# Optimization experiments

Hardware: AMD Instinct MI355X
Metric: run time of the kernel (lower is better)

Reference implementation:

```python
import jax, jax.numpy as jnp
import numpy as np

UNITS = 1024
FORECAST = 128
FEATS = 128
BATCH = 256
WARMUP = 256


def setup_inputs() -> dict:
    key = jax.random.key(0)
    ks = jax.random.split(key, 4)
    s = 0.02  # small init scale to keep gates out of saturation
    return {
        "inputs": jax.random.normal(ks[0], (BATCH, WARMUP, FEATS), jnp.float32),
        "W_i": jax.random.normal(ks[1], (FEATS, 4 * UNITS), jnp.float32) * s,
        "W_h": jax.random.normal(ks[2], (UNITS, 4 * UNITS), jnp.float32) * s,
        "b": jnp.zeros((4 * UNITS,), jnp.float32),
        "W_d": jax.random.normal(ks[3], (UNITS, FEATS), jnp.float32) * s,
        "b_d": jnp.zeros((FEATS,), jnp.float32),
    }


def _lstm_cell(x, h, c, W_i, W_h, b):
    # Keras LSTMCell: gates ordered [input, forget, cell-candidate, output]
    z = x @ W_i + h @ W_h + b  # [B, 4U]
    i, f, g, o = jnp.split(z, 4, axis=-1)
    c_new = jax.nn.sigmoid(f) * c + jax.nn.sigmoid(i) * jnp.tanh(g)
    h_new = jax.nn.sigmoid(o) * jnp.tanh(c_new)
    return h_new, c_new


def reference(inputs, W_i, W_h, b, W_d, b_d):
    B = inputs.shape[0]
    U = W_h.shape[0]
    h0 = jnp.zeros((B, U), inputs.dtype)
    c0 = jnp.zeros((B, U), inputs.dtype)

    # warmup: run LSTM over the input sequence, keep final state
    def warm_step(carry, x_t):
        h, c = carry
        h, c = _lstm_cell(x_t, h, c, W_i, W_h, b)
        return (h, c), None

    (h, c), _ = jax.lax.scan(warm_step, (h0, c0), jnp.swapaxes(inputs, 0, 1))
    pred = h @ W_d + b_d  # first prediction [B, F]

    def fc_step(carry, _):
        h, c, p = carry
        h, c = _lstm_cell(p, h, c, W_i, W_h, b)
        p = h @ W_d + b_d
        return (h, c, p), p

    _, preds_rest = jax.lax.scan(fc_step, (h, c, pred), None, length=FORECAST - 1)
    preds = jnp.concatenate([pred[None], preds_rest], axis=0)  # [T, B, F]
    return jnp.swapaxes(preds, 0, 1)  # [B, T, F]
```

## Files before the change

kernel.cpp:

```cpp
#include <hip/hip_runtime.h>
#include <hip/hip_bf16.h>

#define UNITS 1024
#define FEATS 128
#define NG    4096
#define NSTEP 383
#define HS    262144
#define HSB   524288UL

#define OX   0UL
#define OWH  16777216UL
#define OWI  25165824UL
#define OWF  26214400UL
#define OWD  34603008UL
#define OBR  34865152UL
#define OBF  34881536UL
#define OH0  34897920UL
#define OHP  35422208UL
#define OHC  36470784UL
#define OCNT 68452352UL

typedef __attribute__((ext_vector_type(8))) short bf16x8;
typedef __attribute__((ext_vector_type(4))) float f32x4;
typedef __attribute__((ext_vector_type(4))) int i32x4;
typedef __attribute__((address_space(3))) char lds_char;
typedef __attribute__((address_space(1))) const char glb_char;

__device__ __forceinline__ void gload_lds16(const void* g, void* l) {
    __builtin_amdgcn_global_load_lds((glb_char*)g, (lds_char*)l, 16, 0, 0);
}
__device__ __forceinline__ int llc_load(const int* p) {
    int v;
    asm volatile("global_load_dword %0, %1, off sc0 sc1\n\ts_waitcnt vmcnt(0)"
                 : "=v"(v) : "v"(p) : "memory");
    return v;
}
__device__ __forceinline__ void l2_atomic_inc(int* p) {
    int one = 1;
    asm volatile("global_atomic_add %0, %1, off" :: "v"(p), "v"(one) : "memory");
}
__device__ __forceinline__ int l2_atomic_poll(int* p) {
    int v; int zero = 0;
    asm volatile("global_atomic_add %0, %1, %2, off sc0\n\ts_waitcnt vmcnt(0)"
                 : "=v"(v) : "v"(p), "v"(zero) : "memory");
    return v;
}

#define CFENCE asm volatile("" ::: "memory")
#define VMCNT0 asm volatile("s_waitcnt vmcnt(0)" ::: "memory")
#define L1INV  asm volatile("buffer_inv" ::: "memory")

__device__ __forceinline__ float sigf(float x) { return 1.0f / (1.0f + __expf(-x)); }
__device__ __forceinline__ float tanh_fast(float x) { return 2.0f / (1.0f + __expf(-2.0f * x)) - 1.0f; }

__device__ __forceinline__ int PK(int k) {
    return (k & ~15) | ((k & 3) << 2) | ((k >> 2) & 3);
}

__device__ __forceinline__ __hip_bfloat16* hist_ptr(char* ws, int s) {
    size_t off;
    if (s == 0)        off = OH0;
    else if (s <= 32)  off = OX  + (size_t)(s - 1) * HSB;
    else if (s <= 48)  off = OWH + (size_t)(s - 33) * HSB;
    else if (s <= 50)  off = OWI + (size_t)(s - 49) * HSB;
    else if (s <= 111) off = OHC + (size_t)(s - 51) * HSB;
    else               off = OWF + (size_t)(s - 112) * HSB;
    return (__hip_bfloat16*)(ws + off);
}

__device__ __forceinline__ void llc_sync(int* c, int target) {
    CFENCE;
    __syncthreads();
    if (threadIdx.x == 0) {
        atomicAdd(c, 1);
        while (llc_load(c) < target) __builtin_amdgcn_s_sleep(8);
    }
    __syncthreads();
    CFENCE;
}


__global__ void cvt_bf16(const float* __restrict__ in, __hip_bfloat16* __restrict__ out, int n) {
    int i = (blockIdx.x * blockDim.x + threadIdx.x) * 4;
    if (i >= n) return;
    float4 v = *(const float4*)(in + i);
    union { ushort4 u4; __hip_bfloat16 h[4]; } pk;
    pk.h[0] = __float2bfloat16(v.x);
    pk.h[1] = __float2bfloat16(v.y);
    pk.h[2] = __float2bfloat16(v.z);
    pk.h[3] = __float2bfloat16(v.w);
    *(ushort4*)(out + i) = pk.u4;
}

__global__ void build_whwi(const float* __restrict__ Wh, const float* __restrict__ Wi,
                           __hip_bfloat16* __restrict__ WhR, __hip_bfloat16* __restrict__ WiR) {
    int idx = blockIdx.x * 256 + threadIdx.x;
    int k = idx >> 12, col = idx & 4095;
    int j = ((col & 1023) << 2) | (col >> 10);
    if (k < 1024) WhR[(size_t)j * 1024 + k] = __float2bfloat16(Wh[(size_t)PK(k) * 4096 + col]);
    else          WiR[(size_t)j * 128 + (k - 1024)] = __float2bfloat16(Wi[(size_t)(k - 1024) * 4096 + col]);
}

__global__ void build_wd(const float* __restrict__ Wd, __hip_bfloat16* __restrict__ WdT) {
    int idx = blockIdx.x * 256 + threadIdx.x;
    int f = idx >> 10, k = idx & 1023;
    WdT[(size_t)f * 1024 + k] = __float2bfloat16(Wd[(size_t)PK(k) * 128 + f]);
}

__global__ void build_bias(const float* __restrict__ b, const float* __restrict__ bd,
                           const float* __restrict__ Wi, float* __restrict__ br, float* __restrict__ bf) {
    int j = blockIdx.x * 256 + threadIdx.x;
    int col = ((j & 3) << 10) | (j >> 2);
    float base = b[col];
    br[j] = base;
    float v = base;
    for (int q = 0; q < 128; ++q) v += bd[q] * Wi[(size_t)q * 4096 + col];
    bf[j] = v;
}

__global__ __launch_bounds__(256) void build_wf(const __hip_bfloat16* __restrict__ WhR,
                                                const __hip_bfloat16* __restrict__ WiR,
                                                const float* __restrict__ Wd,
                                                __hip_bfloat16* __restrict__ WfR) {
    const int j0 = blockIdx.x * 64, k0 = blockIdx.y * 64;
    const int tid = threadIdx.x, wave = tid >> 6, lane = tid & 63;
    const int wj = (wave >> 1) * 32, wk = (wave & 1) * 32;
    const int lr = lane & 15, lq = lane >> 4;
    const int TL = ((lr & 3) << 2) | (lr >> 2);
    f32x4 acc[2][2] = {};
    #pragma unroll
    for (int kc = 0; kc < 4; ++kc) {
        bf16x8 dfr[2], ifr[2];
        #pragma unroll
        for (int q2 = 0; q2 < 2; ++q2) {
            const float* p = Wd + (size_t)(k0 + wk + q2 * 16 + TL) * 128 + kc * 32 + lq * 8;
            __hip_bfloat16* dp = (__hip_bfloat16*)&dfr[q2];
            #pragma unroll
            for (int e = 0; e < 8; ++e) dp[e] = __float2bfloat16(p[e]);
            ifr[q2] = *(const bf16x8*)(WiR + (size_t)(j0 + wj + q2 * 16 + lr) * 128 + kc * 32 + lq * 8);
        }
        acc[0][0] = __builtin_amdgcn_mfma_f32_16x16x32_bf16(dfr[0], ifr[0], acc[0][0], 0, 0, 0);
        acc[0][1] = __builtin_amdgcn_mfma_f32_16x16x32_bf16(dfr[0], ifr[1], acc[0][1], 0, 0, 0);
        acc[1][0] = __builtin_amdgcn_mfma_f32_16x16x32_bf16(dfr[1], ifr[0], acc[1][0], 0, 0, 0);
        acc[1][1] = __builtin_amdgcn_mfma_f32_16x16x32_bf16(dfr[1], ifr[1], acc[1][1], 0, 0, 0);
    }
    #pragma unroll
    for (int cf = 0; cf < 2; ++cf)
        #pragma unroll
        for (int rf = 0; rf < 2; ++rf) {
            const int k = k0 + wk + cf * 16 + lq * 4;
            const int j = j0 + wj + rf * 16 + lr;
            const __hip_bfloat16* whp = WhR + (size_t)j * 1024 + k;
            __hip_bfloat16* wfp = WfR + (size_t)j * 1024 + k;
            #pragma unroll
            for (int e = 0; e < 4; ++e)
                wfp[e] = __float2bfloat16(acc[cf][rf][e] + __bfloat162float(whp[e]));
        }
}

__global__ __launch_bounds__(512, 2) void persist(char* ws) {
    const __hip_bfloat16* xb  = (const __hip_bfloat16*)(ws + OX);
    const __hip_bfloat16* whg = (const __hip_bfloat16*)(ws + OWH);
    const __hip_bfloat16* wig = (const __hip_bfloat16*)(ws + OWI);
    const __hip_bfloat16* wfg = (const __hip_bfloat16*)(ws + OWF);
    const float* brg = (const float*)(ws + OBR);
    const float* bfg = (const float*)(ws + OBF);
    __hip_bfloat16* hp0 = (__hip_bfloat16*)(ws + OHP);
    __hip_bfloat16* hp1 = hp0 + HS;

    __shared__ __hip_bfloat16 Als[9][32][128];
    __shared__ float Xl[4][2][4][2][256];
    __shared__ __hip_bfloat16 hTile[32][32];
    __shared__ int claimv[2];
    __shared__ int rdy[16];

    const int tid = threadIdx.x;

    if (tid < 16) rdy[tid] = 0;
    if (tid == 0) {
        unsigned xcd;
        asm volatile("s_getreg_b32 %0, hwreg(HW_REG_XCC_ID, 0, 32)" : "=s"(xcd));
        int* slotc = (int*)(ws + OCNT + 8192);
        int slot = atomicAdd(slotc + (xcd & 7), 1);
        claimv[0] = (int)(xcd & 7);
        claimv[1] = slot & 31;
    }
    __syncthreads();
    const int grp  = claimv[0];
    const int tile = claimv[1];
    const int n0 = tile * 128;
    const int b0 = grp * 32;
    const int ublk = tile * 32;
    int* fbase = (int*)(ws + OCNT + (size_t)grp * 1024);
    int* glc   = (int*)(ws + OCNT + 8320);

    const int wave = tid >> 6, lane = tid & 63;
    const int cq = wave & 1, kh = wave >> 1;
    const int lr = lane & 15, lq = lane >> 4;

    bf16x8 w[4][9];
    #pragma unroll
    for (int tc = 0; tc < 4; ++tc) {
        const size_t row = (size_t)(n0 + cq * 64 + tc * 16 + lr);
        w[tc][0] = *(const bf16x8*)(wig + row * 128 + kh * 32 + lq * 8);
        #pragma unroll
        for (int c = 0; c < 8; ++c)
            w[tc][1 + c] = *(const bf16x8*)(whg + row * 1024 + c * 128 + kh * 32 + lq * 8);
    }
    float4 biasq = *(const float4*)(brg + n0 + cq * 64 + kh * 16 + lq * 4);

    float creg[2] = {0.f, 0.f};

    if (wave == 0) {
        #pragma unroll
        for (int j = 0; j < 8; ++j) {
            const int r32 = j * 4 + lq;
            const int ce = ((lane & 15) ^ (r32 & 15)) << 3;
            gload_lds16(xb + (size_t)(b0 + r32) * 32768 + ce,
                        (char*)&Als[0][0][0] + j * 1024);
        }
    }

    for (int t = 0; t < NSTEP; ++t) {
        const bool fc = (t >= 256);
        const __hip_bfloat16* hsrc = fc ? hist_ptr(ws, t - 256) : ((t & 1) ? hp1 : hp0);
        __hip_bfloat16* hdst = (t >= 255) ? hist_ptr(ws, t - 255) : ((t & 1) ? hp0 : hp1);

        if (t == 256) {
            #pragma unroll
            for (int tc = 0; tc < 4; ++tc) {
                const size_t row = (size_t)(n0 + cq * 64 + tc * 16 + lr);
                #pragma unroll
                for (int c = 0; c < 8; ++c)
                    w[tc][1 + c] = *(const bf16x8*)(wfg + row * 1024 + c * 128 + kh * 32 + lq * 8);
            }
            biasq = *(const float4*)(bfg + n0 + cq * 64 + kh * 16 + lq * 4);
            VMCNT0;
            llc_sync(glc, 256);
        }

        if (t > 0 && lane == 0) {
            int* fl = fbase + wave * 32;
            while (l2_atomic_poll(fl) < 4 * t) __builtin_amdgcn_s_sleep(1);
        }
        L1INV;
        {
            const __hip_bfloat16* srcb = hsrc + (size_t)b0 * 1024 + wave * 128;
            char* dstc = (char*)&Als[1 + wave][0][0];
            #pragma unroll
            for (int j = 0; j < 8; ++j) {
                const int r32 = j * 4 + lq;
                const int ce = ((lane & 15) ^ (r32 & 15)) << 3;
                gload_lds16(srcb + (size_t)r32 * 1024 + ce, dstc + j * 1024);
            }
        }
        VMCNT0;
        __hip_atomic_store(&rdy[wave], t + 1, __ATOMIC_RELEASE, __HIP_MEMORY_SCOPE_WORKGROUP);

        f32x4 acc[4][2] = {};
        const int sc = ((kh * 4 + lq) ^ lr);
        auto wr_ = [&](int p) {
            while (__hip_atomic_load(&rdy[p], __ATOMIC_ACQUIRE, __HIP_MEMORY_SCOPE_WORKGROUP) < t + 1) {}
            __builtin_amdgcn_sched_barrier(0);
        };
        auto mfr = [&](int r) {
            const bf16x8 a0 = *(const bf16x8*)&Als[r][lr][sc * 8];
            const bf16x8 a1 = *(const bf16x8*)&Als[r][lr + 16][sc * 8];
            #pragma unroll
            for (int tc = 0; tc < 4; ++tc) {
                acc[tc][0] = __builtin_amdgcn_mfma_f32_16x16x32_bf16(w[tc][r], a0, acc[tc][0], 0, 0, 0);
                acc[tc][1] = __builtin_amdgcn_mfma_f32_16x16x32_bf16(w[tc][r], a1, acc[tc][1], 0, 0, 0);
            }
        };
        if (!fc) { wr_(0); mfr(0); }
        #pragma unroll
        for (int r = 1; r <= 8; ++r) { wr_(r - 1); mfr(r); }

        #pragma unroll
        for (int tc = 0; tc < 4; ++tc)
            #pragma unroll
            for (int rf = 0; rf < 2; ++rf)
                *(f32x4*)&Xl[kh][cq][tc][rf][lane * 4] = acc[tc][rf];
        __syncthreads();
        #pragma unroll
        for (int rf = 0; rf < 2; ++rf) {
            f32x4 z = {0.f, 0.f, 0.f, 0.f};
            #pragma unroll
            for (int k2 = 0; k2 < 4; ++k2)
                z += *(const f32x4*)&Xl[k2][cq][kh][rf][lane * 4];
            const float zi = z[0] + biasq.x;
            const float zf = z[1] + biasq.y;
            const float zg = z[2] + biasq.z;
            const float zo = z[3] + biasq.w;
            const float cn = sigf(zf) * creg[rf] + sigf(zi) * tanh_fast(zg);
            creg[rf] = cn;
            hTile[rf * 16 + lr][cq * 16 + lq * 4 + kh] = __float2bfloat16(sigf(zo) * tanh_fast(cn));
        }
        __syncthreads();

        if (tid < 128) {
            const int bl = tid >> 2, ch = tid & 3;
            *(i32x4*)(hdst + (size_t)(b0 + bl) * 1024 + ublk + ch * 8) =
                *(const i32x4*)&hTile[bl][ch * 8];
        }
        VMCNT0;
        __syncthreads();
        if (tid == 0) l2_atomic_inc(fbase + (tile >> 2) * 32);

        if (wave == 0 && t + 1 < 256) {
            #pragma unroll
            for (int j = 0; j < 8; ++j) {
                const int r32 = j * 4 + lq;
                const int ce = ((lane & 15) ^ (r32 & 15)) << 3;
                gload_lds16(xb + (size_t)(b0 + r32) * 32768 + (size_t)(t + 1) * 128 + ce,
                            (char*)&Als[0][0][0] + j * 1024);
            }
        }
    }
}

__global__ __launch_bounds__(256) void pgemm(char* ws, float* __restrict__ out,
                                             const float* __restrict__ bd) {
    const int t = blockIdx.x >> 2;
    const int r0 = (blockIdx.x & 3) * 64;
    const int f0 = blockIdx.y * 64;
    const __hip_bfloat16* A = hist_ptr(ws, t);
    const __hip_bfloat16* Bw = (const __hip_bfloat16*)(ws + OWD);

    __shared__ __hip_bfloat16 Al[2][64 * 64];
    __shared__ __hip_bfloat16 Bl[2][64 * 64];

    const int tid = threadIdx.x;
    const int wave = tid >> 6, lane = tid & 63;
    const int whb = (wave >> 1) * 32, wcf = (wave & 1) * 32;
    const int lr = lane & 15, lq = lane >> 4;
    const int l8 = lane >> 3, cb = lane & 7;
    const int gsw = ((cb ^ l8) << 3);
    const int xk = lr & 7;

    f32x4 acc[2][2] = {};
    const int rA0 = whb + lr, rA1 = whb + lr + 16;
    const int rB0 = wcf + lr, rB1 = wcf + lr + 16;

    auto stage = [&](int buf, int k0) {
        #pragma unroll
        for (int l = 0; l < 2; ++l) {
            const int rt = wave * 16 + l * 8;
            const int row = rt + l8;
            gload_lds16(A + (size_t)(r0 + row) * 1024 + k0 + gsw, &Al[buf][rt * 64]);
            gload_lds16(Bw + (size_t)(f0 + row) * 1024 + k0 + gsw, &Bl[buf][rt * 64]);
        }
    };

    stage(0, 0);
    for (int kk = 0; kk < 16; ++kk) {
        const int buf = kk & 1;
        if (kk + 1 < 16) { stage(buf ^ 1, (kk + 1) << 6); asm volatile("s_waitcnt vmcnt(4)" ::: "memory"); }
        else             { VMCNT0; }
        CFENCE; __builtin_amdgcn_s_barrier(); CFENCE;
        #pragma unroll
        for (int ks = 0; ks < 2; ++ks) {
            const int g0 = ((ks * 4 + lq) ^ xk) << 3;
            bf16x8 a0 = *(const bf16x8*)&Al[buf][rA0 * 64 + g0];
            bf16x8 a1 = *(const bf16x8*)&Al[buf][rA1 * 64 + g0];
            bf16x8 w0 = *(const bf16x8*)&Bl[buf][rB0 * 64 + g0];
            bf16x8 w1 = *(const bf16x8*)&Bl[buf][rB1 * 64 + g0];
            acc[0][0] = __builtin_amdgcn_mfma_f32_16x16x32_bf16(w0, a0, acc[0][0], 0, 0, 0);
            acc[0][1] = __builtin_amdgcn_mfma_f32_16x16x32_bf16(w0, a1, acc[0][1], 0, 0, 0);
            acc[1][0] = __builtin_amdgcn_mfma_f32_16x16x32_bf16(w1, a0, acc[1][0], 0, 0, 0);
            acc[1][1] = __builtin_amdgcn_mfma_f32_16x16x32_bf16(w1, a1, acc[1][1], 0, 0, 0);
        }
        CFENCE; __builtin_amdgcn_s_barrier(); CFENCE;
    }
    #pragma unroll
    for (int cf = 0; cf < 2; ++cf) {
        const int fb = f0 + wcf + cf * 16 + lq * 4;
        const float4 b4 = *(const float4*)(bd + fb);
        #pragma unroll
        for (int rf = 0; rf < 2; ++rf) {
            const int b = r0 + whb + rf * 16 + lr;
            float4 o;
            o.x = acc[cf][rf][0] + b4.x;
            o.y = acc[cf][rf][1] + b4.y;
            o.z = acc[cf][rf][2] + b4.z;
            o.w = acc[cf][rf][3] + b4.w;
            *(float4*)(out + (size_t)b * 16384 + (size_t)t * 128 + fb) = o;
        }
    }
}


extern "C" void kernel_launch(void* const* d_in, const int* in_sizes, int n_in,
                              void* d_out, int out_size, void* d_ws, size_t ws_size,
                              hipStream_t stream) {
    const float* inputs = (const float*)d_in[0];
    const float* W_i    = (const float*)d_in[1];
    const float* W_h    = (const float*)d_in[2];
    const float* b      = (const float*)d_in[3];
    const float* W_d    = (const float*)d_in[4];
    const float* b_d    = (const float*)d_in[5];
    float* out = (float*)d_out;
    char* ws = (char*)d_ws;

    (void)hipMemsetAsync(ws + OHP, 0, HSB, stream);
    (void)hipMemsetAsync(ws + OCNT, 0, 16384, stream);

    cvt_bf16<<<8192, 256, 0, stream>>>(inputs, (__hip_bfloat16*)(ws + OX), 256 * 256 * 128);
    build_whwi<<<(1152 * 4096) / 256, 256, 0, stream>>>(
        W_h, W_i, (__hip_bfloat16*)(ws + OWH), (__hip_bfloat16*)(ws + OWI));
    build_wd<<<(128 * 1024) / 256, 256, 0, stream>>>(W_d, (__hip_bfloat16*)(ws + OWD));
    build_bias<<<16, 256, 0, stream>>>(b, b_d, W_i, (float*)(ws + OBR), (float*)(ws + OBF));
    build_wf<<<dim3(64, 16), 256, 0, stream>>>(
        (const __hip_bfloat16*)(ws + OWH), (const __hip_bfloat16*)(ws + OWI),
        W_d, (__hip_bfloat16*)(ws + OWF));

    char* wsp = ws;
    void* ka[] = { &wsp };
    (void)hipLaunchCooperativeKernel((void*)persist, dim3(256), dim3(512), ka, 0, stream);

    pgemm<<<dim3(512, 2), 256, 0, stream>>>(ws, out, b_d);
}
```

Measured before the change: 1.758 ms.

## Split each batch tile into two 16-row halves with separate flags to pipeline

Each workgroup's 32 batch rows are processed as two 16-row halves, each with its own LDS buffer, readiness flags and global completion counters. The second half's hidden-state loads overlap with compute on the first half, and each half's h slice is published as soon as it is done. The x input is now loaded inside the step rather than prefetched a step ahead. The change adds more flag polling, another barrier pair per step and smaller MFMA batches per LDS read, and it reorganizes the counter layout.

Result: slower. 2.735 ms (+55.6%).

```diff
diff --git a/kernel.cpp b/kernel.cpp
--- a/kernel.cpp
+++ b/kernel.cpp
@@ -168,15 +168,15 @@
     __hip_bfloat16* hp0 = (__hip_bfloat16*)(ws + OHP);
     __hip_bfloat16* hp1 = hp0 + HS;
 
-    __shared__ __hip_bfloat16 Als[9][32][128];
-    __shared__ float Xl[4][2][4][2][256];
-    __shared__ __hip_bfloat16 hTile[32][32];
+    __shared__ __hip_bfloat16 Als[2][9][16][128];
+    __shared__ float Xl[4][2][4][256];
+    __shared__ __hip_bfloat16 hTile[2][16][32];
     __shared__ int claimv[2];
-    __shared__ int rdy[16];
+    __shared__ int rdy[2][8];
 
     const int tid = threadIdx.x;
 
-    if (tid < 16) rdy[tid] = 0;
+    if (tid < 16) rdy[tid >> 3][tid & 7] = 0;
     if (tid == 0) {
         unsigned xcd;
         asm volatile("s_getreg_b32 %0, hwreg(HW_REG_XCC_ID, 0, 32)" : "=s"(xcd));
@@ -208,18 +208,10 @@
             w[tc][1 + c] = *(const bf16x8*)(whg + row * 1024 + c * 128 + kh * 32 + lq * 8);
     }
     float4 biasq = *(const float4*)(brg + n0 + cq * 64 + kh * 16 + lq * 4);
-
     float creg[2] = {0.f, 0.f};
 
-    if (wave == 0) {
-        #pragma unroll
-        for (int j = 0; j < 8; ++j) {
-            const int r32 = j * 4 + lq;
-            const int ce = ((lane & 15) ^ (r32 & 15)) << 3;
-            gload_lds16(xb + (size_t)(b0 + r32) * 32768 + ce,
-                        (char*)&Als[0][0][0] + j * 1024);
-        }
-    }
+    const int sr = lane >> 4;
+    const int scol = lane & 15;
 
     for (int t = 0; t < NSTEP; ++t) {
         const bool fc = (t >= 256);
@@ -240,80 +232,112 @@
         }
 
         if (t > 0 && lane == 0) {
-            int* fl = fbase + wave * 32;
-            while (l2_atomic_poll(fl) < 4 * t) __builtin_amdgcn_s_sleep(1);
+            int* f0 = fbase + wave * 16;
+            while (l2_atomic_poll(f0) < 4 * t) __builtin_amdgcn_s_sleep(1);
         }
         L1INV;
         {
-            const __hip_bfloat16* srcb = hsrc + (size_t)b0 * 1024 + wave * 128;
-            char* dstc = (char*)&Als[1 + wave][0][0];
-            #pragma unroll
-            for (int j = 0; j < 8; ++j) {
-                const int r32 = j * 4 + lq;
-                const int ce = ((lane & 15) ^ (r32 & 15)) << 3;
-                gload_lds16(srcb + (size_t)r32 * 1024 + ce, dstc + j * 1024);
-            }
-        }
+            const int b0g = b0;
+            if (!fc && wave == 0) {
+                #pragma unroll
+                for (int j = 0; j < 4; ++j) {
+                    const int row = j * 4 + sr;
+                    const int ce = (scol ^ row) << 3;
+                    gload_lds16(xb + (size_t)(b0g + row) * 32768 + (size_t)t * 128 + ce,
+                                (char*)&Als[0][0][0][0] + j * 1024);
+                }
+            }
+            const __hip_bfloat16* srcb = hsrc + (size_t)b0g * 1024 + wave * 128;
+            #pragma unroll
+            for (int j = 0; j < 4; ++j) {
+                const int row = j * 4 + sr;
+                const int ce = (scol ^ row) << 3;
+                gload_lds16(srcb + (size_t)row * 1024 + ce,
+                            (char*)&Als[0][1 + wave][0][0] + j * 1024);
+            }
+        }
+        if (t > 0 && lane == 0) {
+            int* f1 = fbase + (8 + wave) * 16;
+            while (l2_atomic_poll(f1) < 4 * t) __builtin_amdgcn_s_sleep(1);
+        }
+        {
+            const int b0g = b0 + 16;
+            if (!fc && wave == 0) {
+                #pragma unroll
+                for (int j = 0; j < 4; ++j) {
+                    const int row = j * 4 + sr;
+                    const int ce = (scol ^ row) << 3;
+                    gload_lds16(xb + (size_t)(b0g + row) * 32768 + (size_t)t * 128 + ce,
+                                (char*)&Als[1][0][0][0] + j * 1024);
+                }
+            }
+            const __hip_bfloat16* srcb = hsrc + (size_t)b0g * 1024 + wave * 128;
+            #pragma unroll
+            for (int j = 0; j < 4; ++j) {
+                const int row = j * 4 + sr;
+                const int ce = (scol ^ row) << 3;
+                gload_lds16(srcb + (size_t)row * 1024 + ce,
+                            (char*)&Als[1][1 + wave][0][0] + j * 1024);
+            }
+        }
+        if (wave == 0 && !fc) { asm volatile("s_waitcnt vmcnt(8)" ::: "memory"); }
+        else                  { asm volatile("s_waitcnt vmcnt(4)" ::: "memory"); }
+        __hip_atomic_store(&rdy[0][wave], t + 1, __ATOMIC_RELEASE, __HIP_MEMORY_SCOPE_WORKGROUP);
         VMCNT0;
-        __hip_atomic_store(&rdy[wave], t + 1, __ATOMIC_RELEASE, __HIP_MEMORY_SCOPE_WORKGROUP);
-
-        f32x4 acc[4][2] = {};
+        __hip_atomic_store(&rdy[1][wave], t + 1, __ATOMIC_RELEASE, __HIP_MEMORY_SCOPE_WORKGROUP);
+
         const int sc = ((kh * 4 + lq) ^ lr);
-        auto wr_ = [&](int p) {
-            while (__hip_atomic_load(&rdy[p], __ATOMIC_ACQUIRE, __HIP_MEMORY_SCOPE_WORKGROUP) < t + 1) {}
-            __builtin_amdgcn_sched_barrier(0);
-        };
-        auto mfr = [&](int r) {
-            const bf16x8 a0 = *(const bf16x8*)&Als[r][lr][sc * 8];
-            const bf16x8 a1 = *(const bf16x8*)&Als[r][lr + 16][sc * 8];
-            #pragma unroll
-            for (int tc = 0; tc < 4; ++tc) {
-                acc[tc][0] = __builtin_amdgcn_mfma_f32_16x16x32_bf16(w[tc][r], a0, acc[tc][0], 0, 0, 0);
-                acc[tc][1] = __builtin_amdgcn_mfma_f32_16x16x32_bf16(w[tc][r], a1, acc[tc][1], 0, 0, 0);
-            }
-        };
-        if (!fc) { wr_(0); mfr(0); }
-        #pragma unroll
-        for (int r = 1; r <= 8; ++r) { wr_(r - 1); mfr(r); }
-
-        #pragma unroll
-        for (int tc = 0; tc < 4; ++tc)
-            #pragma unroll
-            for (int rf = 0; rf < 2; ++rf)
-                *(f32x4*)&Xl[kh][cq][tc][rf][lane * 4] = acc[tc][rf];
-        __syncthreads();
-        #pragma unroll
-        for (int rf = 0; rf < 2; ++rf) {
-            f32x4 z = {0.f, 0.f, 0.f, 0.f};
-            #pragma unroll
-            for (int k2 = 0; k2 < 4; ++k2)
-                z += *(const f32x4*)&Xl[k2][cq][kh][rf][lane * 4];
-            const float zi = z[0] + biasq.x;
-            const float zf = z[1] + biasq.y;
-            const float zg = z[2] + biasq.z;
-            const float zo = z[3] + biasq.w;
-            const float cn = sigf(zf) * creg[rf] + sigf(zi) * tanh_fast(zg);
-            creg[rf] = cn;
-            hTile[rf * 16 + lr][cq * 16 + lq * 4 + kh] = __float2bfloat16(sigf(zo) * tanh_fast(cn));
-        }
-        __syncthreads();
-
-        if (tid < 128) {
-            const int bl = tid >> 2, ch = tid & 3;
-            *(i32x4*)(hdst + (size_t)(b0 + bl) * 1024 + ublk + ch * 8) =
-                *(const i32x4*)&hTile[bl][ch * 8];
-        }
-        VMCNT0;
-        __syncthreads();
-        if (tid == 0) l2_atomic_inc(fbase + (tile >> 2) * 32);
-
-        if (wave == 0 && t + 1 < 256) {
-            #pragma unroll
-            for (int j = 0; j < 8; ++j) {
-                const int r32 = j * 4 + lq;
-                const int ce = ((lane & 15) ^ (r32 & 15)) << 3;
-                gload_lds16(xb + (size_t)(b0 + r32) * 32768 + (size_t)(t + 1) * 128 + ce,
-                            (char*)&Als[0][0][0] + j * 1024);
+
+        #pragma unroll
+        for (int g = 0; g < 2; ++g) {
+            {
+                volatile int* vr = &rdy[g][0];
+                for (;;) {
+                    int m = vr[0];
+                    #pragma unroll
+                    for (int i = 1; i < 8; ++i) { int u = vr[i]; m = (u < m) ? u : m; }
+                    if (m >= t + 1) break;
+                }
+                __builtin_amdgcn_sched_barrier(0);
+            }
+            f32x4 acc[4] = {};
+            if (!fc) {
+                const bf16x8 a = *(const bf16x8*)&Als[g][0][lr][sc * 8];
+                #pragma unroll
+                for (int tc = 0; tc < 4; ++tc)
+                    acc[tc] = __builtin_amdgcn_mfma_f32_16x16x32_bf16(w[tc][0], a, acc[tc], 0, 0, 0);
+            }
+            #pragma unroll
+            for (int r = 1; r <= 8; ++r) {
+                const bf16x8 a = *(const bf16x8*)&Als[g][r][lr][sc * 8];
+                #pragma unroll
+                for (int tc = 0; tc < 4; ++tc)
+                    acc[tc] = __builtin_amdgcn_mfma_f32_16x16x32_bf16(w[tc][r], a, acc[tc], 0, 0, 0);
+            }
+            #pragma unroll
+            for (int tc = 0; tc < 4; ++tc)
+                *(f32x4*)&Xl[kh][cq][tc][lane * 4] = acc[tc];
+            __syncthreads();
+            {
+                f32x4 z = *(const f32x4*)&Xl[0][cq][kh][lane * 4];
+                #pragma unroll
+                for (int k2 = 1; k2 < 4; ++k2)
+                    z += *(const f32x4*)&Xl[k2][cq][kh][lane * 4];
+                const float zi = z[0] + biasq.x;
+                const float zf = z[1] + biasq.y;
+                const float zg = z[2] + biasq.z;
+                const float zo = z[3] + biasq.w;
+                const float cn = sigf(zf) * creg[g] + sigf(zi) * tanh_fast(zg);
+                creg[g] = cn;
+                hTile[g][lr][cq * 16 + lq * 4 + kh] = __float2bfloat16(sigf(zo) * tanh_fast(cn));
+            }
+            __syncthreads();
+            if (wave == g) {
+                const int row = lane >> 2, ch = lane & 3;
+                *(i32x4*)(hdst + (size_t)(b0 + g * 16 + row) * 1024 + ublk + ch * 8) =
+                    *(const i32x4*)&hTile[g][row][ch * 8];
+                VMCNT0;
+                if (lane == 0) l2_atomic_inc(fbase + (g * 8 + (tile >> 2)) * 16);
             }
         }
     }
```

## Give each wave full-K gate rows to drop cross-wave LDS reduction

Applied to the files above, without the earlier changes.

Each wave now owns 16 gate rows across the entire K dimension, so it holds 36 weight fragments and accumulates the full dot product in registers. This removes the Xl LDS partial-sum buffer and one workgroup barrier per step. hTile is double-buffered so a single wave can publish h and bump the flag without a trailing barrier. The x-input load moves into the current step and gets its own ready flag, and the spin-wait sleep is removed. The cost is higher register pressure, serialised publishing by one wave, and busier polling.

After: 2.095 ms. 19.2% more time.

```diff
diff --git a/kernel.cpp b/kernel.cpp
--- a/kernel.cpp
+++ b/kernel.cpp
@@ -169,14 +169,13 @@
     __hip_bfloat16* hp1 = hp0 + HS;
 
     __shared__ __hip_bfloat16 Als[9][32][128];
-    __shared__ float Xl[4][2][4][2][256];
-    __shared__ __hip_bfloat16 hTile[32][32];
+    __shared__ __hip_bfloat16 hTile[2][32][32];
     __shared__ int claimv[2];
-    __shared__ int rdy[16];
+    __shared__ int rdy[12];
 
     const int tid = threadIdx.x;
 
-    if (tid < 16) rdy[tid] = 0;
+    if (tid < 12) rdy[tid] = 0;
     if (tid == 0) {
         unsigned xcd;
         asm volatile("s_getreg_b32 %0, hwreg(HW_REG_XCC_ID, 0, 32)" : "=s"(xcd));
@@ -195,31 +194,24 @@
     int* glc   = (int*)(ws + OCNT + 8320);
 
     const int wave = tid >> 6, lane = tid & 63;
-    const int cq = wave & 1, kh = wave >> 1;
     const int lr = lane & 15, lq = lane >> 4;
 
-    bf16x8 w[4][9];
+    const size_t wrow = (size_t)(n0 + wave * 16 + lr);
+    bf16x8 wv[36];
     #pragma unroll
-    for (int tc = 0; tc < 4; ++tc) {
-        const size_t row = (size_t)(n0 + cq * 64 + tc * 16 + lr);
-        w[tc][0] = *(const bf16x8*)(wig + row * 128 + kh * 32 + lq * 8);
-        #pragma unroll
-        for (int c = 0; c < 8; ++c)
-            w[tc][1 + c] = *(const bf16x8*)(whg + row * 1024 + c * 128 + kh * 32 + lq * 8);
-    }
-    float4 biasq = *(const float4*)(brg + n0 + cq * 64 + kh * 16 + lq * 4);
-
+    for (int s = 0; s < 4; ++s)
+        wv[s] = *(const bf16x8*)(wig + wrow * 128 + s * 32 + lq * 8);
+    #pragma unroll
+    for (int c = 0; c < 8; ++c)
+        #pragma unroll
+        for (int s = 0; s < 4; ++s)
+            wv[4 + 4 * c + s] = *(const bf16x8*)(whg + wrow * 1024 + c * 128 + s * 32 + lq * 8);
+    float4 biasq = *(const float4*)(brg + n0 + wave * 16 + lq * 4);
     float creg[2] = {0.f, 0.f};
 
-    if (wave == 0) {
-        #pragma unroll
-        for (int j = 0; j < 8; ++j) {
-            const int r32 = j * 4 + lq;
-            const int ce = ((lane & 15) ^ (r32 & 15)) << 3;
-            gload_lds16(xb + (size_t)(b0 + r32) * 32768 + ce,
-                        (char*)&Als[0][0][0] + j * 1024);
-        }
-    }
+    const int sr = lane >> 4;
+    const int scol = lane & 15;
+    const int upos = ((wave >> 2) << 4) | (lq << 2) | (wave & 3);
 
     for (int t = 0; t < NSTEP; ++t) {
         const bool fc = (t >= 256);
@@ -228,20 +220,18 @@
 
         if (t == 256) {
             #pragma unroll
-            for (int tc = 0; tc < 4; ++tc) {
-                const size_t row = (size_t)(n0 + cq * 64 + tc * 16 + lr);
+            for (int c = 0; c < 8; ++c)
                 #pragma unroll
-                for (int c = 0; c < 8; ++c)
-                    w[tc][1 + c] = *(const bf16x8*)(wfg + row * 1024 + c * 128 + kh * 32 + lq * 8);
-            }
-            biasq = *(const float4*)(bfg + n0 + cq * 64 + kh * 16 + lq * 4);
+                for (int s = 0; s < 4; ++s)
+                    wv[4 + 4 * c + s] = *(const bf16x8*)(wfg + wrow * 1024 + c * 128 + s * 32 + lq * 8);
+            biasq = *(const float4*)(bfg + n0 + wave * 16 + lq * 4);
             VMCNT0;
             llc_sync(glc, 256);
         }
 
         if (t > 0 && lane == 0) {
             int* fl = fbase + wave * 32;
-            while (l2_atomic_poll(fl) < 4 * t) __builtin_amdgcn_s_sleep(1);
+            while (l2_atomic_poll(fl) < 4 * t) { }
         }
         L1INV;
         {
@@ -249,72 +239,82 @@
             char* dstc = (char*)&Als[1 + wave][0][0];
             #pragma unroll
             for (int j = 0; j < 8; ++j) {
-                const int r32 = j * 4 + lq;
-                const int ce = ((lane & 15) ^ (r32 & 15)) << 3;
-                gload_lds16(srcb + (size_t)r32 * 1024 + ce, dstc + j * 1024);
-            }
-        }
-        VMCNT0;
-        __hip_atomic_store(&rdy[wave], t + 1, __ATOMIC_RELEASE, __HIP_MEMORY_SCOPE_WORKGROUP);
-
-        f32x4 acc[4][2] = {};
-        const int sc = ((kh * 4 + lq) ^ lr);
-        auto wr_ = [&](int p) {
-            while (__hip_atomic_load(&rdy[p], __ATOMIC_ACQUIRE, __HIP_MEMORY_SCOPE_WORKGROUP) < t + 1) {}
+                const int row = j * 4 + sr;
+                const int ce = (scol ^ (row & 15)) << 3;
+                gload_lds16(srcb + (size_t)row * 1024 + ce, dstc + j * 1024);
+            }
+        }
+        if (wave == 0) {
+            if (!fc) {
+                #pragma unroll
+                for (int j = 0; j < 8; ++j) {
+                    const int row = j * 4 + sr;
+                    const int ce = (scol ^ (row & 15)) << 3;
+                    gload_lds16(xb + (size_t)(b0 + row) * 32768 + (size_t)t * 128 + ce,
+                                (char*)&Als[0][0][0] + j * 1024);
+                }
+                asm volatile("s_waitcnt vmcnt(8)" ::: "memory");
+                __hip_atomic_store(&rdy[0], t + 1, __ATOMIC_RELEASE, __HIP_MEMORY_SCOPE_WORKGROUP);
+                VMCNT0;
+                __hip_atomic_store(&rdy[8], t + 1, __ATOMIC_RELEASE, __HIP_MEMORY_SCOPE_WORKGROUP);
+            } else {
+                VMCNT0;
+                __hip_atomic_store(&rdy[0], t + 1, __ATOMIC_RELEASE, __HIP_MEMORY_SCOPE_WORKGROUP);
+            }
+        } else {
+            VMCNT0;
+            __hip_atomic_store(&rdy[wave], t + 1, __ATOMIC_RELEASE, __HIP_MEMORY_SCOPE_WORKGROUP);
+        }
+
+        f32x4 acc[2][2] = {};
+        auto gate = [&](int idx) {
+            while (__hip_atomic_load(&rdy[idx], __ATOMIC_ACQUIRE, __HIP_MEMORY_SCOPE_WORKGROUP) < t + 1) {}
             __builtin_amdgcn_sched_barrier(0);
         };
-        auto mfr = [&](int r) {
-            const bf16x8 a0 = *(const bf16x8*)&Als[r][lr][sc * 8];
-            const bf16x8 a1 = *(const bf16x8*)&Als[r][lr + 16][sc * 8];
-            #pragma unroll
-            for (int tc = 0; tc < 4; ++tc) {
-                acc[tc][0] = __builtin_amdgcn_mfma_f32_16x16x32_bf16(w[tc][r], a0, acc[tc][0], 0, 0, 0);
-                acc[tc][1] = __builtin_amdgcn_mfma_f32_16x16x32_bf16(w[tc][r], a1, acc[tc][1], 0, 0, 0);
+        auto chunk = [&](int r, int wbase) {
+            #pragma unroll
+            for (int s = 0; s < 4; ++s) {
+                const int sc = ((s * 4 + lq) ^ lr) << 3;
+                const bf16x8 a0 = *(const bf16x8*)&Als[r][lr][sc];
+                const bf16x8 a1 = *(const bf16x8*)&Als[r][lr + 16][sc];
+                acc[0][s & 1] = __builtin_amdgcn_mfma_f32_16x16x32_bf16(wv[wbase + s], a0, acc[0][s & 1], 0, 0, 0);
+                acc[1][s & 1] = __builtin_amdgcn_mfma_f32_16x16x32_bf16(wv[wbase + s], a1, acc[1][s & 1], 0, 0, 0);
             }
         };
-        if (!fc) { wr_(0); mfr(0); }
-        #pragma unroll
-        for (int r = 1; r <= 8; ++r) { wr_(r - 1); mfr(r); }
-
-        #pragma unroll
-        for (int tc = 0; tc < 4; ++tc)
-            #pragma unroll
-            for (int rf = 0; rf < 2; ++rf)
-                *(f32x4*)&Xl[kh][cq][tc][rf][lane * 4] = acc[tc][rf];
+        #pragma unroll
+        for (int c = 0; c < 8; ++c) { gate(c); chunk(1 + c, 4 + 4 * c); }
+        if (!fc) { gate(8); chunk(0, 0); }
+
+        {
+            const f32x4 z0 = acc[0][0] + acc[0][1];
+            const f32x4 z1 = acc[1][0] + acc[1][1];
+            {
+                const float zi = z0[0] + biasq.x, zf = z0[1] + biasq.y;
+                const float zg = z0[2] + biasq.z, zo = z0[3] + biasq.w;
+                const float cn = sigf(zf) * creg[0] + sigf(zi) * tanh_fast(zg);
+                creg[0] = cn;
+                hTile[t & 1][lr][upos] = __float2bfloat16(sigf(zo) * tanh_fast(cn));
+            }
+            {
+                const float zi = z1[0] + biasq.x, zf = z1[1] + biasq.y;
+                const float zg = z1[2] + biasq.z, zo = z1[3] + biasq.w;
+                const float cn = sigf(zf) * creg[1] + sigf(zi) * tanh_fast(zg);
+                creg[1] = cn;
+                hTile[t & 1][16 + lr][upos] = __float2bfloat16(sigf(zo) * tanh_fast(cn));
+            }
+        }
         __syncthreads();
-        #pragma unroll
-        for (int rf = 0; rf < 2; ++rf) {
-            f32x4 z = {0.f, 0.f, 0.f, 0.f};
-            #pragma unroll
-            for (int k2 = 0; k2 < 4; ++k2)
-                z += *(const f32x4*)&Xl[k2][cq][kh][rf][lane * 4];
-            const float zi = z[0] + biasq.x;
-            const float zf = z[1] + biasq.y;
-            const float zg = z[2] + biasq.z;
-            const float zo = z[3] + biasq.w;
-            const float cn = sigf(zf) * creg[rf] + sigf(zi) * tanh_fast(zg);
-            creg[rf] = cn;
-            hTile[rf * 16 + lr][cq * 16 + lq * 4 + kh] = __float2bfloat16(sigf(zo) * tanh_fast(cn));
-        }
-        __syncthreads();
-
-        if (tid < 128) {
-            const int bl = tid >> 2, ch = tid & 3;
-            *(i32x4*)(hdst + (size_t)(b0 + bl) * 1024 + ublk + ch * 8) =
-                *(const i32x4*)&hTile[bl][ch * 8];
-        }
-        VMCNT0;
-        __syncthreads();
-        if (tid == 0) l2_atomic_inc(fbase + (tile >> 2) * 32);
-
-        if (wave == 0 && t + 1 < 256) {
-            #pragma unroll
-            for (int j = 0; j < 8; ++j) {
-                const int r32 = j * 4 + lq;
-                const int ce = ((lane & 15) ^ (r32 & 15)) << 3;
-                gload_lds16(xb + (size_t)(b0 + r32) * 32768 + (size_t)(t + 1) * 128 + ce,
-                            (char*)&Als[0][0][0] + j * 1024);
-            }
+
+        if (wave == 7) {
+            #pragma unroll
+            for (int i = 0; i < 2; ++i) {
+                const int q = lane + i * 64;
+                const int row = q >> 2, ch = q & 3;
+                *(i32x4*)(hdst + (size_t)(b0 + row) * 1024 + ublk + ch * 8) =
+                    *(const i32x4*)&hTile[t & 1][row][ch * 8];
+            }
+            VMCNT0;
+            if (lane == 0) l2_atomic_inc(fbase + (tile >> 2) * 32);
         }
     }
 }
```

## Give each consumer tile its own readiness flags and split publish across waves

Applied to the files above, without the earlier changes.

The cross-block step flags change from one shared counter per chunk and batch group to one counter per (consumer tile, chunk). Producers fan their increments out to all 32 consumers, so pollers on a group no longer contend on the same counter, and the polling loop drops its sleep. The h-tile store and flag update move to waves 6-7 with no trailing workgroup barrier, and h loads use an sc0 cache hint. The x-input gate gets its own LDS ready slot. This trades 32x more atomic increments per tile for less contention on each counter and lower wake-up latency, and it enlarges the counter memset.

Result: no change. 1.749 ms, median of 2 (-0.5%).

```diff
diff --git a/kernel.cpp b/kernel.cpp
--- a/kernel.cpp
+++ b/kernel.cpp
@@ -28,6 +28,9 @@
 
 __device__ __forceinline__ void gload_lds16(const void* g, void* l) {
     __builtin_amdgcn_global_load_lds((glb_char*)g, (lds_char*)l, 16, 0, 0);
+}
+__device__ __forceinline__ void gload_lds16_sc0(const void* g, void* l) {
+    __builtin_amdgcn_global_load_lds((glb_char*)g, (lds_char*)l, 16, 0, 1);
 }
 __device__ __forceinline__ int llc_load(const int* p) {
     int v;
@@ -172,15 +175,15 @@
     __shared__ float Xl[4][2][4][2][256];
     __shared__ __hip_bfloat16 hTile[32][32];
     __shared__ int claimv[2];
-    __shared__ int rdy[16];
+    __shared__ int rdy[12];
 
     const int tid = threadIdx.x;
 
-    if (tid < 16) rdy[tid] = 0;
+    if (tid < 12) rdy[tid] = 0;
     if (tid == 0) {
         unsigned xcd;
         asm volatile("s_getreg_b32 %0, hwreg(HW_REG_XCC_ID, 0, 32)" : "=s"(xcd));
-        int* slotc = (int*)(ws + OCNT + 8192);
+        int* slotc = (int*)(ws + OCNT + 262144);
         int slot = atomicAdd(slotc + (xcd & 7), 1);
         claimv[0] = (int)(xcd & 7);
         claimv[1] = slot & 31;
@@ -191,8 +194,11 @@
     const int n0 = tile * 128;
     const int b0 = grp * 32;
     const int ublk = tile * 32;
-    int* fbase = (int*)(ws + OCNT + (size_t)grp * 1024);
-    int* glc   = (int*)(ws + OCNT + 8320);
+    int* flg = (int*)(ws + OCNT);
+    int* glc = (int*)(ws + OCNT + 262144 + 128);
+    auto flag_at = [&](int cons, int chunk) {
+        return flg + ((size_t)(grp * 32 + cons) * 8 + chunk) * 32;
+    };
 
     const int wave = tid >> 6, lane = tid & 63;
     const int cq = wave & 1, kh = wave >> 1;
@@ -208,15 +214,17 @@
             w[tc][1 + c] = *(const bf16x8*)(whg + row * 1024 + c * 128 + kh * 32 + lq * 8);
     }
     float4 biasq = *(const float4*)(brg + n0 + cq * 64 + kh * 16 + lq * 4);
-
     float creg[2] = {0.f, 0.f};
 
+    const int sr = lane >> 4;
+    const int scol = lane & 15;
+
     if (wave == 0) {
         #pragma unroll
         for (int j = 0; j < 8; ++j) {
-            const int r32 = j * 4 + lq;
-            const int ce = ((lane & 15) ^ (r32 & 15)) << 3;
-            gload_lds16(xb + (size_t)(b0 + r32) * 32768 + ce,
+            const int row = j * 4 + sr;
+            const int ce = (scol ^ (row & 15)) << 3;
+            gload_lds16(xb + (size_t)(b0 + row) * 32768 + ce,
                         (char*)&Als[0][0][0] + j * 1024);
         }
     }
@@ -240,8 +248,8 @@
         }
 
         if (t > 0 && lane == 0) {
-            int* fl = fbase + wave * 32;
-            while (l2_atomic_poll(fl) < 4 * t) __builtin_amdgcn_s_sleep(1);
+            int* fl = flag_at(tile, wave);
+            while (l2_atomic_poll(fl) < 8 * t) { }
         }
         L1INV;
         {
@@ -249,20 +257,22 @@
             char* dstc = (char*)&Als[1 + wave][0][0];
             #pragma unroll
             for (int j = 0; j < 8; ++j) {
-                const int r32 = j * 4 + lq;
-                const int ce = ((lane & 15) ^ (r32 & 15)) << 3;
-                gload_lds16(srcb + (size_t)r32 * 1024 + ce, dstc + j * 1024);
+                const int row = j * 4 + sr;
+                const int ce = (scol ^ (row & 15)) << 3;
+                gload_lds16_sc0(srcb + (size_t)row * 1024 + ce, dstc + j * 1024);
             }
         }
         VMCNT0;
         __hip_atomic_store(&rdy[wave], t + 1, __ATOMIC_RELEASE, __HIP_MEMORY_SCOPE_WORKGROUP);
+        if (wave == 0 && !fc)
+            __hip_atomic_store(&rdy[8], t + 1, __ATOMIC_RELEASE, __HIP_MEMORY_SCOPE_WORKGROUP);
 
         f32x4 acc[4][2] = {};
-        const int sc = ((kh * 4 + lq) ^ lr);
-        auto wr_ = [&](int p) {
-            while (__hip_atomic_load(&rdy[p], __ATOMIC_ACQUIRE, __HIP_MEMORY_SCOPE_WORKGROUP) < t + 1) {}
+        auto gate = [&](int idx) {
+            while (__hip_atomic_load(&rdy[idx], __ATOMIC_ACQUIRE, __HIP_MEMORY_SCOPE_WORKGROUP) < t + 1) {}
             __builtin_amdgcn_sched_barrier(0);
         };
+        const int sc = ((kh * 4 + lq) ^ lr);
         auto mfr = [&](int r) {
             const bf16x8 a0 = *(const bf16x8*)&Als[r][lr][sc * 8];
             const bf16x8 a1 = *(const bf16x8*)&Als[r][lr + 16][sc * 8];
@@ -272,9 +282,9 @@
                 acc[tc][1] = __builtin_amdgcn_mfma_f32_16x16x32_bf16(w[tc][r], a1, acc[tc][1], 0, 0, 0);
             }
         };
-        if (!fc) { wr_(0); mfr(0); }
-        #pragma unroll
-        for (int r = 1; r <= 8; ++r) { wr_(r - 1); mfr(r); }
+        if (!fc) { gate(8); mfr(0); }
+        #pragma unroll
+        for (int r = 1; r <= 8; ++r) { gate(r - 1); mfr(r); }
 
         #pragma unroll
         for (int tc = 0; tc < 4; ++tc)
@@ -298,21 +308,20 @@
         }
         __syncthreads();
 
-        if (tid < 128) {
-            const int bl = tid >> 2, ch = tid & 3;
-            *(i32x4*)(hdst + (size_t)(b0 + bl) * 1024 + ublk + ch * 8) =
-                *(const i32x4*)&hTile[bl][ch * 8];
-        }
-        VMCNT0;
-        __syncthreads();
-        if (tid == 0) l2_atomic_inc(fbase + (tile >> 2) * 32);
-
+        if (wave >= 6) {
+            const int q = (wave - 6) * 64 + lane;
+            const int row = q >> 2, ch = q & 3;
+            *(i32x4*)(hdst + (size_t)(b0 + row) * 1024 + ublk + ch * 8) =
+                *(const i32x4*)&hTile[row][ch * 8];
+            VMCNT0;
+            if (lane < 32) l2_atomic_inc(flag_at(lane, tile >> 2));
+        }
         if (wave == 0 && t + 1 < 256) {
             #pragma unroll
             for (int j = 0; j < 8; ++j) {
-                const int r32 = j * 4 + lq;
-                const int ce = ((lane & 15) ^ (r32 & 15)) << 3;
-                gload_lds16(xb + (size_t)(b0 + r32) * 32768 + (size_t)(t + 1) * 128 + ce,
+                const int row = j * 4 + sr;
+                const int ce = (scol ^ (row & 15)) << 3;
+                gload_lds16(xb + (size_t)(b0 + row) * 32768 + (size_t)(t + 1) * 128 + ce,
                             (char*)&Als[0][0][0] + j * 1024);
             }
         }
@@ -403,7 +412,7 @@
     char* ws = (char*)d_ws;
 
     (void)hipMemsetAsync(ws + OHP, 0, HSB, stream);
-    (void)hipMemsetAsync(ws + OCNT, 0, 16384, stream);
+    (void)hipMemsetAsync(ws + OCNT, 0, 262400, stream);
 
     cvt_bf16<<<8192, 256, 0, stream>>>(inputs, (__hip_bfloat16*)(ws + OX), 256 * 256 * 128);
     build_whwi<<<(1152 * 4096) / 256, 256, 0, stream>>>(
```
